# Optimization experiments

Hardware: AMD Instinct MI355X
Metric: run time of the kernel (lower is better)

The kernel has to match this reference:

```python
import jax, jax.numpy as jnp
import numpy as np

B, T, S, U = 64, 64, 128, 4  # batch, frames, yt_img_size, upscale_factor
P, U2 = S * S, U * U          # per-pixel batch dim, tiny-matmul output dim
RECON = S * U                 # 512


def setup_inputs() -> dict:
    key = jax.random.key(0)
    k1, k2, k3 = jax.random.split(key, 3)
    yt = jax.random.normal(k1, (B, T, S, S), dtype=jnp.float32)
    weights = jax.random.normal(k2, (P, T, U2), dtype=jnp.float32)
    biases = jax.random.normal(k3, (P, 1, U2), dtype=jnp.float32)
    return {"yt": yt, "weights": weights, "biases": biases}


def reference(yt, weights, biases):
    # (B, T, S, S) -> (P, B, T): one tiny (B,T)x(T,U2) GEMM per pixel location
    y = yt.reshape(B, T, P).transpose(2, 0, 1)
    # per-location batched matmul + bias: (P, B, U2)
    up = jnp.einsum('pbt,ptu->pbu', y, weights) + biases
    # pixel-shuffle style upsampling: (S, S, B, U, U) -> (B, S, U, S, U) -> (B, 1, 512, 512)
    up = up.reshape(S, S, B, U, U).transpose(2, 0, 3, 1, 4)
    out = up.reshape(B, RECON, RECON)[:, None, :, :]
    # seq_block is identity in this configuration
    return out
```

## Files before the change

kernel.cpp:

```cpp
#include <hip/hip_runtime.h>

namespace {
constexpr int Sdim = 128;
constexpr int Tdim = 64;
constexpr int U2c  = 16;
constexpr int PT   = 32;
constexpr int NTHREADS = 512;
constexpr int PP = Sdim * Sdim;
constexpr int TQ = 16;
constexpr int NSTG = Tdim / TQ;

typedef float floatx4 __attribute__((ext_vector_type(4)));
}

__global__ __launch_bounds__(NTHREADS, 2)
void upscale_fused(const float* __restrict__ yt,
                   const float* __restrict__ wgt,
                   const float* __restrict__ bias,
                   float* __restrict__ out)
{
    __shared__ float wlds[TQ * U2c * PT];

    const int tid   = threadIdx.x;
    const int p_blk = blockIdx.x * PT;

    const int pg = tid & 15;
    const int b2 = (tid >> 4) & 31;
    const int p0 = p_blk + pg * 2;

    const float4* wgt4 = reinterpret_cast<const float4*>(wgt);

    float4 sreg[4];
    auto stage_load = [&](int stg) {
        #pragma unroll
        for (int i = 0; i < 4; ++i) {
            const int f = i * NTHREADS + tid;
            const int r = f >> 6;
            const int c = f & 63;
            sreg[i] = wgt4[(size_t)(p_blk + r) * 256 + (size_t)stg * 64 + c];
        }
    };
    auto stage_write = [&]() {
        #pragma unroll
        for (int i = 0; i < 4; ++i) {
            const int f = i * NTHREADS + tid;
            const int r = f >> 6;
            const int c = f & 63;
            const int tw = c >> 2;
            const int uq = c & 3;
            const int col = r ^ (2 * tw);
            float* dst = &wlds[(tw * U2c + uq * 4) * PT + col];
            dst[0 * PT] = sreg[i].x;  dst[1 * PT] = sreg[i].y;
            dst[2 * PT] = sreg[i].z;  dst[3 * PT] = sreg[i].w;
        }
    };

    stage_load(0);

    float acc[2][2][16];
    #pragma unroll
    for (int jp = 0; jp < 2; ++jp) {
        const float* bp = bias + (size_t)(p0 + jp) * U2c;
        const float4 q0 = *reinterpret_cast<const float4*>(bp + 0);
        const float4 q1 = *reinterpret_cast<const float4*>(bp + 4);
        const float4 q2 = *reinterpret_cast<const float4*>(bp + 8);
        const float4 q3 = *reinterpret_cast<const float4*>(bp + 12);
        const float bb[16] = {q0.x,q0.y,q0.z,q0.w, q1.x,q1.y,q1.z,q1.w,
                              q2.x,q2.y,q2.z,q2.w, q3.x,q3.y,q3.z,q3.w};
        #pragma unroll
        for (int u = 0; u < 16; ++u) { acc[0][jp][u] = bb[u]; acc[1][jp][u] = bb[u]; }
    }

    const float* y0b = yt + (size_t)b2 * ((size_t)Tdim * PP) + p0;
    const float* y1b = y0b + (size_t)32 * Tdim * PP;
    auto ldy = [&](int t, float2& a, float2& b) {
        a = *reinterpret_cast<const float2*>(y0b + (size_t)t * PP);
        b = *reinterpret_cast<const float2*>(y1b + (size_t)t * PP);
    };

    auto step = [&](const float2& ya, const float2& yb, int tl) {
        const float* wrow = &wlds[tl * (U2c * PT) + ((pg * 2) ^ (2 * tl))];
        #pragma unroll
        for (int u = 0; u < 16; ++u) {
            const float2 wv = *reinterpret_cast<const float2*>(wrow + u * PT);
            acc[0][0][u] = fmaf(ya.x, wv.x, acc[0][0][u]);
            acc[0][1][u] = fmaf(ya.y, wv.y, acc[0][1][u]);
            acc[1][0][u] = fmaf(yb.x, wv.x, acc[1][0][u]);
            acc[1][1][u] = fmaf(yb.y, wv.y, acc[1][1][u]);
        }
    };

    float2 A0, A1, B0, B1, C0, C1, D0, D1;
    ldy(0, A0, A1); ldy(1, B0, B1); ldy(2, C0, C1); ldy(3, D0, D1);

    stage_write();
    __syncthreads();

    #pragma unroll 1
    for (int stg = 0; stg < NSTG; ++stg) {
        if (stg + 1 < NSTG) stage_load(stg + 1);

        #pragma unroll 1
        for (int tq = 0; tq < TQ; tq += 4) {
            const int tg = stg * TQ + tq;
            step(A0, A1, tq + 0); { const int tf = (tg + 4 < Tdim) ? tg + 4 : Tdim - 1; ldy(tf, A0, A1); }
            step(B0, B1, tq + 1); { const int tf = (tg + 5 < Tdim) ? tg + 5 : Tdim - 1; ldy(tf, B0, B1); }
            step(C0, C1, tq + 2); { const int tf = (tg + 6 < Tdim) ? tg + 6 : Tdim - 1; ldy(tf, C0, C1); }
            step(D0, D1, tq + 3); { const int tf = (tg + 7 < Tdim) ? tg + 7 : Tdim - 1; ldy(tf, D0, D1); }
        }

        if (stg + 1 < NSTG) {
            __syncthreads();
            stage_write();
            __syncthreads();
        }
    }

    const int s1   = p_blk / Sdim;
    const int s2_0 = p_blk % Sdim;

    #pragma unroll
    for (int bi = 0; bi < 2; ++bi) {
        const int b = b2 + bi * 32;
        float* ob = out + (size_t)b * (512 * 512);
        #pragma unroll
        for (int jp = 0; jp < 2; ++jp) {
            const int c0 = (s2_0 + pg * 2 + jp) * 4;
            #pragma unroll
            for (int u1 = 0; u1 < 4; ++u1) {
                const int r = s1 * 4 + u1;
                floatx4 v;
                v.x = acc[bi][jp][u1 * 4 + 0];
                v.y = acc[bi][jp][u1 * 4 + 1];
                v.z = acc[bi][jp][u1 * 4 + 2];
                v.w = acc[bi][jp][u1 * 4 + 3];
                __builtin_nontemporal_store(v, reinterpret_cast<floatx4*>(ob + (size_t)r * 512 + c0));
            }
        }
    }
}

extern "C" void kernel_launch(void* const* d_in, const int* in_sizes, int n_in,
                              void* d_out, int out_size, void* d_ws, size_t ws_size,
                              hipStream_t stream)
{
    const float* yt   = (const float*)d_in[0];
    const float* wgt  = (const float*)d_in[1];
    const float* bias = (const float*)d_in[2];
    float* outp       = (float*)d_out;

    dim3 grid(PP / PT);
    dim3 block(NTHREADS);
    hipLaunchKernelGGL(upscale_fused, grid, block, 0, stream, yt, wgt, bias, outp);
}
```

Baseline: 109.9 us.

## Remap threads to 4 pixels x 1 batch, double-buffer weight LDS stages

```diff
diff --git a/kernel.cpp b/kernel.cpp
--- a/kernel.cpp
+++ b/kernel.cpp
@@ -19,14 +19,14 @@
                    const float* __restrict__ bias,
                    float* __restrict__ out)
 {
-    __shared__ float wlds[TQ * U2c * PT];
+    __shared__ float wlds[2][TQ * U2c * PT];
 
     const int tid   = threadIdx.x;
     const int p_blk = blockIdx.x * PT;
 
-    const int pg = tid & 15;
-    const int b2 = (tid >> 4) & 31;
-    const int p0 = p_blk + pg * 2;
+    const int pg = tid & 7;
+    const int bb = tid >> 3;
+    const int p0 = p_blk + pg * 4;
 
     const float4* wgt4 = reinterpret_cast<const float4*>(wgt);
 
@@ -40,7 +40,7 @@
             sreg[i] = wgt4[(size_t)(p_blk + r) * 256 + (size_t)stg * 64 + c];
         }
     };
-    auto stage_write = [&]() {
+    auto stage_write = [&](int buf) {
         #pragma unroll
         for (int i = 0; i < 4; ++i) {
             const int f = i * NTHREADS + tid;
@@ -48,8 +48,8 @@
             const int c = f & 63;
             const int tw = c >> 2;
             const int uq = c & 3;
-            const int col = r ^ (2 * tw);
-            float* dst = &wlds[(tw * U2c + uq * 4) * PT + col];
+            const int col = r ^ (4 * (tw & 7));
+            float* dst = &wlds[buf][(tw * U2c + uq * 4) * PT + col];
             dst[0 * PT] = sreg[i].x;  dst[1 * PT] = sreg[i].y;
             dst[2 * PT] = sreg[i].z;  dst[3 * PT] = sreg[i].w;
         }
@@ -57,85 +57,75 @@
 
     stage_load(0);
 
-    float acc[2][2][16];
+    float acc[4][16];
     #pragma unroll
-    for (int jp = 0; jp < 2; ++jp) {
-        const float* bp = bias + (size_t)(p0 + jp) * U2c;
-        const float4 q0 = *reinterpret_cast<const float4*>(bp + 0);
-        const float4 q1 = *reinterpret_cast<const float4*>(bp + 4);
-        const float4 q2 = *reinterpret_cast<const float4*>(bp + 8);
-        const float4 q3 = *reinterpret_cast<const float4*>(bp + 12);
-        const float bb[16] = {q0.x,q0.y,q0.z,q0.w, q1.x,q1.y,q1.z,q1.w,
-                              q2.x,q2.y,q2.z,q2.w, q3.x,q3.y,q3.z,q3.w};
+    for (int j = 0; j < 4; ++j) {
+        const float* bp = bias + (size_t)(p0 + j) * U2c;
         #pragma unroll
-        for (int u = 0; u < 16; ++u) { acc[0][jp][u] = bb[u]; acc[1][jp][u] = bb[u]; }
+        for (int q = 0; q < 4; ++q) {
+            const float4 v = *reinterpret_cast<const float4*>(bp + q * 4);
+            acc[j][q * 4 + 0] = v.x;  acc[j][q * 4 + 1] = v.y;
+            acc[j][q * 4 + 2] = v.z;  acc[j][q * 4 + 3] = v.w;
+        }
     }
 
-    const float* y0b = yt + (size_t)b2 * ((size_t)Tdim * PP) + p0;
-    const float* y1b = y0b + (size_t)32 * Tdim * PP;
-    auto ldy = [&](int t, float2& a, float2& b) {
-        a = *reinterpret_cast<const float2*>(y0b + (size_t)t * PP);
-        b = *reinterpret_cast<const float2*>(y1b + (size_t)t * PP);
+    const float* yb = yt + (size_t)bb * ((size_t)Tdim * PP) + p0;
+    auto ldy = [&](int t) {
+        return *reinterpret_cast<const float4*>(yb + (size_t)t * PP);
     };
 
-    auto step = [&](const float2& ya, const float2& yb, int tl) {
-        const float* wrow = &wlds[tl * (U2c * PT) + ((pg * 2) ^ (2 * tl))];
+    auto step = [&](const float4& y, int buf, int tl) {
+        const float* wbase = &wlds[buf][(size_t)tl * (U2c * PT) + ((pg * 4) ^ (4 * (tl & 7)))];
         #pragma unroll
         for (int u = 0; u < 16; ++u) {
-            const float2 wv = *reinterpret_cast<const float2*>(wrow + u * PT);
-            acc[0][0][u] = fmaf(ya.x, wv.x, acc[0][0][u]);
-            acc[0][1][u] = fmaf(ya.y, wv.y, acc[0][1][u]);
-            acc[1][0][u] = fmaf(yb.x, wv.x, acc[1][0][u]);
-            acc[1][1][u] = fmaf(yb.y, wv.y, acc[1][1][u]);
+            const float4 wv = *reinterpret_cast<const float4*>(wbase + u * PT);
+            acc[0][u] = fmaf(y.x, wv.x, acc[0][u]);
+            acc[1][u] = fmaf(y.y, wv.y, acc[1][u]);
+            acc[2][u] = fmaf(y.z, wv.z, acc[2][u]);
+            acc[3][u] = fmaf(y.w, wv.w, acc[3][u]);
         }
     };
 
-    float2 A0, A1, B0, B1, C0, C1, D0, D1;
-    ldy(0, A0, A1); ldy(1, B0, B1); ldy(2, C0, C1); ldy(3, D0, D1);
+    float4 A = ldy(0), B = ldy(1), C = ldy(2), D = ldy(3);
 
-    stage_write();
+    stage_write(0);
     __syncthreads();
 
     #pragma unroll 1
     for (int stg = 0; stg < NSTG; ++stg) {
-        if (stg + 1 < NSTG) stage_load(stg + 1);
-
+        const int buf = stg & 1;
         #pragma unroll 1
         for (int tq = 0; tq < TQ; tq += 4) {
             const int tg = stg * TQ + tq;
-            step(A0, A1, tq + 0); { const int tf = (tg + 4 < Tdim) ? tg + 4 : Tdim - 1; ldy(tf, A0, A1); }
-            step(B0, B1, tq + 1); { const int tf = (tg + 5 < Tdim) ? tg + 5 : Tdim - 1; ldy(tf, B0, B1); }
-            step(C0, C1, tq + 2); { const int tf = (tg + 6 < Tdim) ? tg + 6 : Tdim - 1; ldy(tf, C0, C1); }
-            step(D0, D1, tq + 3); { const int tf = (tg + 7 < Tdim) ? tg + 7 : Tdim - 1; ldy(tf, D0, D1); }
+            step(A, buf, tq + 0); if (tg + 4 < Tdim) A = ldy(tg + 4);
+            step(B, buf, tq + 1); if (tg + 5 < Tdim) B = ldy(tg + 5);
+            step(C, buf, tq + 2); if (tg + 6 < Tdim) C = ldy(tg + 6);
+            step(D, buf, tq + 3); if (tg + 7 < Tdim) D = ldy(tg + 7);
+            if (tq == 0 && stg + 1 < NSTG) stage_load(stg + 1);
         }
-
         if (stg + 1 < NSTG) {
-            __syncthreads();
-            stage_write();
+            stage_write(buf ^ 1);
             __syncthreads();
         }
     }
 
-    const int s1   = p_blk / Sdim;
-    const int s2_0 = p_blk % Sdim;
+    const int s1    = p_blk / Sdim;
+    const int s2_0  = p_blk % Sdim;
+    const int cbase = (s2_0 + pg * 4) * 4;
+    float* ob = out + (size_t)bb * (512 * 512);
 
     #pragma unroll
-    for (int bi = 0; bi < 2; ++bi) {
-        const int b = b2 + bi * 32;
-        float* ob = out + (size_t)b * (512 * 512);
+    for (int u1 = 0; u1 < 4; ++u1) {
+        const int r = s1 * 4 + u1;
+        float* rp = ob + (size_t)r * 512 + cbase;
         #pragma unroll
-        for (int jp = 0; jp < 2; ++jp) {
-            const int c0 = (s2_0 + pg * 2 + jp) * 4;
-            #pragma unroll
-            for (int u1 = 0; u1 < 4; ++u1) {
-                const int r = s1 * 4 + u1;
-                floatx4 v;
-                v.x = acc[bi][jp][u1 * 4 + 0];
-                v.y = acc[bi][jp][u1 * 4 + 1];
-                v.z = acc[bi][jp][u1 * 4 + 2];
-                v.w = acc[bi][jp][u1 * 4 + 3];
-                __builtin_nontemporal_store(v, reinterpret_cast<floatx4*>(ob + (size_t)r * 512 + c0));
-            }
+        for (int j = 0; j < 4; ++j) {
+            floatx4 v;
+            v.x = acc[j][u1 * 4 + 0];
+            v.y = acc[j][u1 * 4 + 1];
+            v.z = acc[j][u1 * 4 + 2];
+            v.w = acc[j][u1 * 4 + 3];
+            __builtin_nontemporal_store(v, reinterpret_cast<floatx4*>(rp + j * 4));
         }
     }
 }
```

After: 145.3 us. 1.32x slower.
